# Kernel optimization log

Hardware: AMD Instinct MI355X
Metric: run time of the kernel (lower is better)

## Reference

```python
import jax, jax.numpy as jnp
import numpy as np

HID = 512
BATCH = 64
SRC_LEN = 2048


def setup_inputs() -> dict:
    key = jax.random.key(0)
    ks = jax.random.split(key, 8)
    s = 1.0 / np.sqrt(HID)
    return {
        "h": jax.random.normal(ks[0], (1, BATCH, HID), dtype=jnp.float32),
        "enc_out": jax.random.normal(ks[1], (BATCH, SRC_LEN, HID), dtype=jnp.float32),
        "W1_w": jax.random.uniform(ks[2], (HID, HID), jnp.float32, -s, s),
        "W1_b": jax.random.uniform(ks[3], (HID,), jnp.float32, -s, s),
        "W2_w": jax.random.uniform(ks[4], (HID, HID), jnp.float32, -s, s),
        "W2_b": jax.random.uniform(ks[5], (HID,), jnp.float32, -s, s),
        "V_w": jax.random.uniform(ks[6], (1, HID), jnp.float32, -s, s),
        "V_b": jax.random.uniform(ks[7], (1,), jnp.float32, -s, s),
    }


def reference(h, enc_out, W1_w, W1_b, W2_w, W2_b, V_w, V_b):
    # h: [1, B, H] -> [B, 1, H]; broadcast against enc_out: [B, S, H]
    h_b = jnp.transpose(h, (1, 0, 2))                       # [B, 1, H]
    proj_enc = jnp.einsum('bsh,oh->bso', enc_out, W1_w) + W1_b  # [B, S, H]
    proj_h = jnp.einsum('bqh,oh->bqo', h_b, W2_w) + W2_b        # [B, 1, H]
    energy = jnp.tanh(proj_enc + proj_h)                        # [B, S, H]
    scores = jnp.einsum('bsh,oh->bso', energy, V_w)[..., 0] + V_b[0]  # [B, S]
    return jax.nn.softmax(scores, axis=1)
```

## Files before the change

kernel.cpp:

```cpp
#include <hip/hip_runtime.h>
#include <hip/hip_bf16.h>

#define HID   512
#define BATCH 64
#define SRC   2048
#define MROWS (BATCH * SRC)

typedef __bf16 bf16x8 __attribute__((ext_vector_type(8)));
typedef __bf16 bf16x4 __attribute__((ext_vector_type(4)));
typedef float  f32x16 __attribute__((ext_vector_type(16)));

__device__ inline float fast_tanh(float x) {
    float e = __builtin_amdgcn_exp2f(x * 2.8853900817779268f);
    return 1.0f - 2.0f * __builtin_amdgcn_rcpf(e + 1.0f);
}

__global__ void cvt_w1(const float* __restrict__ W1w, __bf16* __restrict__ W1bf) {
    int i = (blockIdx.x * 256 + threadIdx.x) * 4;
    float4 v = *(const float4*)(W1w + i);
    bf16x4 o;
    o[0] = (__bf16)v.x; o[1] = (__bf16)v.y; o[2] = (__bf16)v.z; o[3] = (__bf16)v.w;
    *(bf16x4*)(W1bf + i) = o;
}

__global__ void prep_bias(const float* __restrict__ h, const float* __restrict__ W2w,
                          const float* __restrict__ W2b, const float* __restrict__ W1b,
                          float* __restrict__ biasc) {
    int b = blockIdx.x;
    int tid = threadIdx.x;
    __shared__ float hh[HID];
    hh[tid]       = h[b * HID + tid];
    hh[tid + 256] = h[b * HID + tid + 256];
    __syncthreads();
    const float4* h4 = (const float4*)hh;
    for (int o = tid; o < HID; o += 256) {
        const float4* w4 = (const float4*)(W2w + (size_t)o * HID);
        float s = 0.f;
        #pragma unroll 8
        for (int k = 0; k < HID / 4; ++k) {
            float4 a = h4[k]; float4 w = w4[k];
            s += a.x * w.x + a.y * w.y + a.z * w.z + a.w * w.w;
        }
        biasc[b * HID + o] = s + W2b[o] + W1b[o];
    }
}

__global__ __launch_bounds__(512, 2) void attn_main(
        const float* __restrict__ enc, const __bf16* __restrict__ W1bf,
        const float* __restrict__ biasc, const float* __restrict__ Vw,
        float* __restrict__ scores) {
    __shared__ __bf16 Abuf[2 * 2 * 512];
    __shared__ __bf16 Bbuf[16 * 2 * 512];
    __shared__ float bias_lds[HID];
    __shared__ float vw_lds[HID];
    __shared__ float sred[2][4][32];

    const int tid = threadIdx.x;
    const int blockRow = blockIdx.x * 64;
    const int b = blockIdx.x >> 5;

    bias_lds[tid] = biasc[b * HID + tid];
    vw_lds[tid]   = Vw[tid];

    const int am  = tid >> 3;
    const int akk = (tid & 7) * 4;
    const float* gA = enc + (size_t)(blockRow + am) * HID + akk;
    {
    }
    const int apanel = akk >> 4;
    const int ahalf  = (akk >> 3) & 1;
    const int aj0    = akk & 7;
    const int a_w_off = (((am >> 5) * 2 + apanel) * 512) + ((am & 31) + 32 * ahalf) * 8 + aj0;

    int b_w_off[4];
    const __bf16* gB[4];
    #pragma unroll
    for (int i = 0; i < 4; ++i) {
        int c = tid + 512 * i;
        int o = c >> 2, sub = c & 3, p = sub >> 1, hf = sub & 1;
        b_w_off[i] = ((o >> 5) * 2 + p) * 512 + ((o & 31) + 32 * hf) * 8;
        gB[i] = W1bf + (size_t)o * HID + p * 16 + hf * 8;
    }

    const int lane = tid & 63;
    const int wave = tid >> 6;
    const int wm = wave >> 2;
    const int wo = wave & 3;
    const int a_r_off = (wm * 2) * 512 + lane * 8;
    const int b_r_off = (wo * 4) * 2 * 512 + lane * 8;

    f32x16 acc[4];
    #pragma unroll
    for (int t = 0; t < 4; ++t)
        #pragma unroll
        for (int i = 0; i < 16; ++i) acc[t][i] = 0.f;

    for (int kt = 0; kt < 16; ++kt) {
        float4 av = *(const float4*)gA; gA += 32;
        bf16x8 bv[4];
        #pragma unroll
        for (int i = 0; i < 4; ++i) { bv[i] = *(const bf16x8*)gB[i]; gB[i] += 32; }
        bf16x4 ab;
        ab[0] = (__bf16)av.x; ab[1] = (__bf16)av.y; ab[2] = (__bf16)av.z; ab[3] = (__bf16)av.w;

        __syncthreads();
        *(bf16x4*)&Abuf[a_w_off] = ab;
        #pragma unroll
        for (int i = 0; i < 4; ++i) *(bf16x8*)&Bbuf[b_w_off[i]] = bv[i];
        __syncthreads();

        bf16x8 a0 = *(const bf16x8*)&Abuf[a_r_off];
        bf16x8 a1 = *(const bf16x8*)&Abuf[a_r_off + 512];
        #pragma unroll
        for (int ot = 0; ot < 4; ++ot) {
            bf16x8 b0 = *(const bf16x8*)&Bbuf[b_r_off + ot * 1024];
            bf16x8 b1 = *(const bf16x8*)&Bbuf[b_r_off + ot * 1024 + 512];
            acc[ot] = __builtin_amdgcn_mfma_f32_32x32x16_bf16(a0, b0, acc[ot], 0, 0, 0);
            acc[ot] = __builtin_amdgcn_mfma_f32_32x32x16_bf16(a1, b1, acc[ot], 0, 0, 0);
        }
    }

    float partial[16];
    #pragma unroll
    for (int r = 0; r < 16; ++r) partial[r] = 0.f;
    const int col = lane & 31;
    const int hfi = lane >> 5;
    #pragma unroll
    for (int ot = 0; ot < 4; ++ot) {
        int o = wo * 128 + ot * 32 + col;
        float bb = bias_lds[o];
        float vv = vw_lds[o];
        #pragma unroll
        for (int r = 0; r < 16; ++r) {
            float e = fast_tanh(acc[ot][r] + bb);
            partial[r] += e * vv;
        }
    }
    #pragma unroll
    for (int m = 1; m <= 16; m <<= 1)
        #pragma unroll
        for (int r = 0; r < 16; ++r) partial[r] += __shfl_xor(partial[r], m, 64);

    if (col == 0) {
        #pragma unroll
        for (int r = 0; r < 16; ++r) {
            int rl = (r & 3) + 8 * (r >> 2) + 4 * hfi;
            sred[wm][wo][rl] = partial[r];
        }
    }
    __syncthreads();
    if (tid < 64) {
        int wmx = tid >> 5, rl = tid & 31;
        float s = sred[wmx][0][rl] + sred[wmx][1][rl] + sred[wmx][2][rl] + sred[wmx][3][rl];
        scores[blockRow + wmx * 32 + rl] = s;
    }
}

__global__ void softmax_k(float* __restrict__ scores) {
    int b = blockIdx.x;
    int tid = threadIdx.x;
    int lane = tid & 63, wv = tid >> 6;
    __shared__ float red[4];
    float* row = scores + (size_t)b * SRC;
    float4 v0 = *(float4*)(row + tid * 8);
    float4 v1 = *(float4*)(row + tid * 8 + 4);
    float x[8] = {v0.x, v0.y, v0.z, v0.w, v1.x, v1.y, v1.z, v1.w};
    float mx = x[0];
    #pragma unroll
    for (int r = 1; r < 8; ++r) mx = fmaxf(mx, x[r]);
    #pragma unroll
    for (int m = 1; m <= 32; m <<= 1) mx = fmaxf(mx, __shfl_xor(mx, m, 64));
    if (lane == 0) red[wv] = mx;
    __syncthreads();
    mx = fmaxf(fmaxf(red[0], red[1]), fmaxf(red[2], red[3]));
    __syncthreads();
    float s = 0.f;
    #pragma unroll
    for (int r = 0; r < 8; ++r) {
        x[r] = __builtin_amdgcn_exp2f((x[r] - mx) * 1.44269504088896f);
        s += x[r];
    }
    #pragma unroll
    for (int m = 1; m <= 32; m <<= 1) s += __shfl_xor(s, m, 64);
    if (lane == 0) red[wv] = s;
    __syncthreads();
    s = red[0] + red[1] + red[2] + red[3];
    float inv = 1.0f / s;
    float4 o0 = make_float4(x[0] * inv, x[1] * inv, x[2] * inv, x[3] * inv);
    float4 o1 = make_float4(x[4] * inv, x[5] * inv, x[6] * inv, x[7] * inv);
    *(float4*)(row + tid * 8)     = o0;
    *(float4*)(row + tid * 8 + 4) = o1;
}

extern "C" void kernel_launch(void* const* d_in, const int* in_sizes, int n_in,
                              void* d_out, int out_size, void* d_ws, size_t ws_size,
                              hipStream_t stream) {
    const float* h    = (const float*)d_in[0];
    const float* enc  = (const float*)d_in[1];
    const float* W1w  = (const float*)d_in[2];
    const float* W1b  = (const float*)d_in[3];
    const float* W2w  = (const float*)d_in[4];
    const float* W2b  = (const float*)d_in[5];
    const float* Vw   = (const float*)d_in[6];
    float* out = (float*)d_out;

    __bf16* W1bf = (__bf16*)d_ws;
    float*  biasc = (float*)((char*)d_ws + HID * HID * sizeof(__bf16));

    cvt_w1   <<<(HID * HID) / (256 * 4), 256, 0, stream>>>(W1w, W1bf);
    prep_bias<<<BATCH, 256, 0, stream>>>(h, W2w, W2b, W1b, biasc);
    attn_main<<<MROWS / 64, 512, 0, stream>>>(enc, W1bf, biasc, Vw, out);
    softmax_k<<<BATCH, 256, 0, stream>>>(out);
}
```

Measured before the change: 505.7 us.

## Stage whole A tile in padded LDS and stream pre-packed W1 from global

The W1 weight is pre-packed into MFMA fragment order, so each wave loads its B operands straight from global/L2 with a one-step register prefetch and never stages them in LDS. The full 64x512 enc tile is converted to bf16 once into a padded LDS buffer, and the per-k-step double __syncthreads loop is removed. Each wave now covers all 64 rows and 64 output columns with four accumulators, and the final reduction runs over eight waves. This aims to cut barrier and LDS staging overhead and to allow more resident blocks, at the cost of about 66KB of LDS per block and heavier global traffic for W1.

```diff
diff --git a/kernel.cpp b/kernel.cpp
--- a/kernel.cpp
+++ b/kernel.cpp
@@ -10,17 +10,26 @@
 typedef __bf16 bf16x4 __attribute__((ext_vector_type(4)));
 typedef float  f32x16 __attribute__((ext_vector_type(16)));
 
+#define PANEL 520
+
 __device__ inline float fast_tanh(float x) {
     float e = __builtin_amdgcn_exp2f(x * 2.8853900817779268f);
     return 1.0f - 2.0f * __builtin_amdgcn_rcpf(e + 1.0f);
 }
 
-__global__ void cvt_w1(const float* __restrict__ W1w, __bf16* __restrict__ W1bf) {
-    int i = (blockIdx.x * 256 + threadIdx.x) * 4;
-    float4 v = *(const float4*)(W1w + i);
-    bf16x4 o;
-    o[0] = (__bf16)v.x; o[1] = (__bf16)v.y; o[2] = (__bf16)v.z; o[3] = (__bf16)v.w;
-    *(bf16x4*)(W1bf + i) = o;
+__global__ void pack_w1(const float* __restrict__ W1w, __bf16* __restrict__ Bpk) {
+    int t = blockIdx.x * 256 + threadIdx.x;
+    int l = t & 63, tile = t >> 6;
+    int ot = tile & 15, kt = tile >> 4;
+    int o = ot * 32 + (l & 31);
+    int k = kt * 16 + (l >> 5) * 8;
+    const float* src = W1w + (size_t)o * HID + k;
+    float4 v0 = *(const float4*)src;
+    float4 v1 = *(const float4*)(src + 4);
+    bf16x8 r;
+    r[0]=(__bf16)v0.x; r[1]=(__bf16)v0.y; r[2]=(__bf16)v0.z; r[3]=(__bf16)v0.w;
+    r[4]=(__bf16)v1.x; r[5]=(__bf16)v1.y; r[6]=(__bf16)v1.z; r[7]=(__bf16)v1.w;
+    ((bf16x8*)Bpk)[t] = r;
 }
 
 __global__ void prep_bias(const float* __restrict__ h, const float* __restrict__ W2w,
@@ -45,114 +54,93 @@
     }
 }
 
-__global__ __launch_bounds__(512, 2) void attn_main(
-        const float* __restrict__ enc, const __bf16* __restrict__ W1bf,
+__global__ __launch_bounds__(512, 4) void attn_main(
+        const float* __restrict__ enc, const __bf16* __restrict__ Bpk,
         const float* __restrict__ biasc, const float* __restrict__ Vw,
         float* __restrict__ scores) {
-    __shared__ __bf16 Abuf[2 * 2 * 512];
-    __shared__ __bf16 Bbuf[16 * 2 * 512];
-    __shared__ float bias_lds[HID];
-    __shared__ float vw_lds[HID];
-    __shared__ float sred[2][4][32];
+    __shared__ __bf16 AL[64 * PANEL];
+    __shared__ float sred[64][9];
 
     const int tid = threadIdx.x;
     const int blockRow = blockIdx.x * 64;
     const int b = blockIdx.x >> 5;
-
-    bias_lds[tid] = biasc[b * HID + tid];
-    vw_lds[tid]   = Vw[tid];
-
-    const int am  = tid >> 3;
-    const int akk = (tid & 7) * 4;
-    const float* gA = enc + (size_t)(blockRow + am) * HID + akk;
-    {
-    }
-    const int apanel = akk >> 4;
-    const int ahalf  = (akk >> 3) & 1;
-    const int aj0    = akk & 7;
-    const int a_w_off = (((am >> 5) * 2 + apanel) * 512) + ((am & 31) + 32 * ahalf) * 8 + aj0;
-
-    int b_w_off[4];
-    const __bf16* gB[4];
-    #pragma unroll
-    for (int i = 0; i < 4; ++i) {
-        int c = tid + 512 * i;
-        int o = c >> 2, sub = c & 3, p = sub >> 1, hf = sub & 1;
-        b_w_off[i] = ((o >> 5) * 2 + p) * 512 + ((o & 31) + 32 * hf) * 8;
-        gB[i] = W1bf + (size_t)o * HID + p * 16 + hf * 8;
-    }
-
     const int lane = tid & 63;
-    const int wave = tid >> 6;
-    const int wm = wave >> 2;
-    const int wo = wave & 3;
-    const int a_r_off = (wm * 2) * 512 + lane * 8;
-    const int b_r_off = (wo * 4) * 2 * 512 + lane * 8;
-
-    f32x16 acc[4];
-    #pragma unroll
-    for (int t = 0; t < 4; ++t)
-        #pragma unroll
-        for (int i = 0; i < 16; ++i) acc[t][i] = 0.f;
-
-    for (int kt = 0; kt < 16; ++kt) {
-        float4 av = *(const float4*)gA; gA += 32;
-        bf16x8 bv[4];
-        #pragma unroll
-        for (int i = 0; i < 4; ++i) { bv[i] = *(const bf16x8*)gB[i]; gB[i] += 32; }
-        bf16x4 ab;
-        ab[0] = (__bf16)av.x; ab[1] = (__bf16)av.y; ab[2] = (__bf16)av.z; ab[3] = (__bf16)av.w;
-
-        __syncthreads();
-        *(bf16x4*)&Abuf[a_w_off] = ab;
-        #pragma unroll
-        for (int i = 0; i < 4; ++i) *(bf16x8*)&Bbuf[b_w_off[i]] = bv[i];
-        __syncthreads();
-
-        bf16x8 a0 = *(const bf16x8*)&Abuf[a_r_off];
-        bf16x8 a1 = *(const bf16x8*)&Abuf[a_r_off + 512];
-        #pragma unroll
-        for (int ot = 0; ot < 4; ++ot) {
-            bf16x8 b0 = *(const bf16x8*)&Bbuf[b_r_off + ot * 1024];
-            bf16x8 b1 = *(const bf16x8*)&Bbuf[b_r_off + ot * 1024 + 512];
-            acc[ot] = __builtin_amdgcn_mfma_f32_32x32x16_bf16(a0, b0, acc[ot], 0, 0, 0);
-            acc[ot] = __builtin_amdgcn_mfma_f32_32x32x16_bf16(a1, b1, acc[ot], 0, 0, 0);
-        }
-    }
-
-    float partial[16];
-    #pragma unroll
-    for (int r = 0; r < 16; ++r) partial[r] = 0.f;
+    const int wv = tid >> 6;
     const int col = lane & 31;
     const int hfi = lane >> 5;
-    #pragma unroll
-    for (int ot = 0; ot < 4; ++ot) {
-        int o = wo * 128 + ot * 32 + col;
-        float bb = bias_lds[o];
-        float vv = vw_lds[o];
+
+    const int o0 = (2 * wv) * 32 + col;
+    const int o1 = o0 + 32;
+    float bb0 = biasc[b * HID + o0], bb1 = biasc[b * HID + o1];
+    float vv0 = Vw[o0],               vv1 = Vw[o1];
+
+    const float4* encB = (const float4*)enc + (size_t)blockRow * 128;
+    #pragma unroll
+    for (int i = 0; i < 16; ++i) {
+        int f = i * 512 + tid;
+        float4 v = encB[f];
+        int row = f >> 7;
+        int kq  = (f & 127) << 2;
+        int kt = kq >> 4, half = (kq >> 3) & 1, j = kq & 7;
+        int off = (kt * 2 + (row >> 5)) * PANEL + ((row & 31) + 32 * half) * 8 + j;
+        bf16x4 o4;
+        o4[0]=(__bf16)v.x; o4[1]=(__bf16)v.y; o4[2]=(__bf16)v.z; o4[3]=(__bf16)v.w;
+        *(bf16x4*)&AL[off] = o4;
+    }
+    __syncthreads();
+
+    const bf16x8* pB0 = (const bf16x8*)Bpk + (size_t)(2 * wv) * 64 + lane;
+    const bf16x8* pB1 = pB0 + 64;
+    const __bf16* pA  = AL + lane * 8;
+
+    f32x16 acc00, acc01, acc10, acc11;
+    #pragma unroll
+    for (int i = 0; i < 16; ++i) { acc00[i]=0.f; acc01[i]=0.f; acc10[i]=0.f; acc11[i]=0.f; }
+
+    bf16x8 b0 = pB0[0];
+    bf16x8 b1 = pB1[0];
+    #pragma unroll 4
+    for (int kt = 0; kt < 32; ++kt) {
+        int nk = (kt < 31) ? (kt + 1) : 31;
+        bf16x8 nb0 = pB0[(size_t)nk * 1024];
+        bf16x8 nb1 = pB1[(size_t)nk * 1024];
+        bf16x8 a0 = *(const bf16x8*)(pA + kt * (2 * PANEL));
+        bf16x8 a1 = *(const bf16x8*)(pA + kt * (2 * PANEL) + PANEL);
+        acc00 = __builtin_amdgcn_mfma_f32_32x32x16_bf16(a0, b0, acc00, 0, 0, 0);
+        acc10 = __builtin_amdgcn_mfma_f32_32x32x16_bf16(a1, b0, acc10, 0, 0, 0);
+        acc01 = __builtin_amdgcn_mfma_f32_32x32x16_bf16(a0, b1, acc01, 0, 0, 0);
+        acc11 = __builtin_amdgcn_mfma_f32_32x32x16_bf16(a1, b1, acc11, 0, 0, 0);
+        b0 = nb0; b1 = nb1;
+    }
+
+    float p0[16], p1[16];
+    #pragma unroll
+    for (int r = 0; r < 16; ++r) {
+        p0[r] = vv0 * fast_tanh(acc00[r] + bb0) + vv1 * fast_tanh(acc01[r] + bb1);
+        p1[r] = vv0 * fast_tanh(acc10[r] + bb0) + vv1 * fast_tanh(acc11[r] + bb1);
+    }
+    #pragma unroll
+    for (int m = 1; m <= 16; m <<= 1) {
         #pragma unroll
         for (int r = 0; r < 16; ++r) {
-            float e = fast_tanh(acc[ot][r] + bb);
-            partial[r] += e * vv;
+            p0[r] += __shfl_xor(p0[r], m, 64);
+            p1[r] += __shfl_xor(p1[r], m, 64);
         }
     }
-    #pragma unroll
-    for (int m = 1; m <= 16; m <<= 1)
-        #pragma unroll
-        for (int r = 0; r < 16; ++r) partial[r] += __shfl_xor(partial[r], m, 64);
-
     if (col == 0) {
         #pragma unroll
         for (int r = 0; r < 16; ++r) {
             int rl = (r & 3) + 8 * (r >> 2) + 4 * hfi;
-            sred[wm][wo][rl] = partial[r];
+            sred[rl][wv]      = p0[r];
+            sred[32 + rl][wv] = p1[r];
         }
     }
     __syncthreads();
     if (tid < 64) {
-        int wmx = tid >> 5, rl = tid & 31;
-        float s = sred[wmx][0][rl] + sred[wmx][1][rl] + sred[wmx][2][rl] + sred[wmx][3][rl];
-        scores[blockRow + wmx * 32 + rl] = s;
+        float s = 0.f;
+        #pragma unroll
+        for (int w = 0; w < 8; ++w) s += sred[tid][w];
+        scores[blockRow + tid] = s;
     }
 }
 
@@ -204,11 +192,11 @@
     const float* Vw   = (const float*)d_in[6];
     float* out = (float*)d_out;
 
-    __bf16* W1bf = (__bf16*)d_ws;
+    __bf16* Bpk  = (__bf16*)d_ws;
     float*  biasc = (float*)((char*)d_ws + HID * HID * sizeof(__bf16));
 
-    cvt_w1   <<<(HID * HID) / (256 * 4), 256, 0, stream>>>(W1w, W1bf);
+    pack_w1  <<<128, 256, 0, stream>>>(W1w, Bpk);
     prep_bias<<<BATCH, 256, 0, stream>>>(h, W2w, W2b, W1b, biasc);
-    attn_main<<<MROWS / 64, 512, 0, stream>>>(enc, W1bf, biasc, Vw, out);
+    attn_main<<<MROWS / 64, 512, 0, stream>>>(enc, Bpk, biasc, Vw, out);
     softmax_k<<<BATCH, 256, 0, stream>>>(out);
 }
```

New measurement: 491.5 us. 2.8% less time.
